# Performance work log

Hardware: AMD Instinct MI355X
Metric: run time of the kernel (lower is better)

## Reference

```python
import jax, jax.numpy as jnp
from jax import lax
import numpy as np

V, H = 512, 512


def gru_cell(x, h, Wih, Whh, bih, bhh):
    # PyTorch GRUCell: r,z,n gate order
    gi = x @ Wih.T + bih
    gh = h @ Whh.T + bhh
    ir, iz, inn = jnp.split(gi, 3, axis=-1)
    hr, hz, hn = jnp.split(gh, 3, axis=-1)
    r = jax.nn.sigmoid(ir + hr)
    z = jax.nn.sigmoid(iz + hz)
    n = jnp.tanh(inn + r * hn)
    return (1.0 - z) * n + z * h


def setup_inputs() -> dict:
    key = jax.random.key(0)
    ks = jax.random.split(key, 20)
    S, T, B = 200, 200, 256
    w = lambda k, shape: (jax.random.normal(k, shape, jnp.float32) * 0.05)
    inp = {
        "input_seq": jax.random.randint(ks[0], (S, B), 0, V),
        "input_len": jax.random.randint(ks[1], (B,), 1, S + 1),
        "target_seq": jax.random.randint(ks[2], (T, B), 0, V),
        "enc_embed": w(ks[3], (V, H)),
        "enc_Wih": w(ks[4], (3 * H, H)),
        "enc_Whh": w(ks[5], (3 * H, H)),
        "enc_bih": w(ks[6], (3 * H,)),
        "enc_bhh": w(ks[7], (3 * H,)),
        "att_W": w(ks[8], (H, H)),
        "att_b": w(ks[9], (H,)),
        "dec_embed": w(ks[10], (V, H)),
        "dec_Wih": w(ks[11], (3 * H, H)),
        "dec_Whh": w(ks[12], (3 * H, H)),
        "dec_bih": w(ks[13], (3 * H,)),
        "dec_bhh": w(ks[14], (3 * H,)),
        "mlp_W": w(ks[15], (H, 2 * H)),
        "mlp_b": w(ks[16], (H,)),
        "out_W": w(ks[17], (V, H)),
        "out_b": w(ks[18], (V,)),
    }
    return inp


def reference(input_seq, input_len, target_seq, enc_embed, enc_Wih, enc_Whh,
              enc_bih, enc_bhh, att_W, att_b, dec_embed, dec_Wih, dec_Whh,
              dec_bih, dec_bhh, mlp_W, mlp_b, out_W, out_b):
    S, B = input_seq.shape
    T = target_seq.shape[0]

    # ---- Encoder: length-masked GRU (equivalent to pack/pad) ----
    xs = enc_embed[input_seq]                              # (S,B,H)
    mask = jnp.arange(S)[:, None] < input_len[None, :]     # (S,B)
    h0 = jnp.zeros((B, H), xs.dtype)

    def estep(h, inp):
        x, m = inp
        m = m[:, None]
        hn = gru_cell(x, h, enc_Wih, enc_Whh, enc_bih, enc_bhh)
        h = jnp.where(m, hn, h)
        return h, jnp.where(m, h, 0.0)                     # padded outputs are zero

    h_enc, enc_out = lax.scan(estep, h0, (xs, mask))       # h_enc (B,H), enc_out (S,B,H)

    # ---- Decoder: teacher forcing (training path) ----
    dec_tokens = jnp.concatenate(
        [jnp.ones((1, B), target_seq.dtype), target_seq[:-1]], axis=0)  # start token 1
    dec_emb = dec_embed[dec_tokens]                        # (T,B,H)

    def dstep(h, emb_t):
        ah = jax.nn.relu(h @ att_W.T + att_b)              # (B,H)
        e = jnp.einsum('sbh,bh->bs', enc_out, ah)          # additive-style score
        att = jax.nn.softmax(e, axis=1)                    # (B,S)
        ctx = jnp.einsum('sbh,bs->bh', enc_out, att)       # (B,H)
        x = jnp.tanh(jnp.concatenate([emb_t, ctx], axis=1) @ mlp_W.T + mlp_b)
        hn = gru_cell(x, h, dec_Wih, dec_Whh, dec_bih, dec_bhh)
        dist = jax.nn.softmax(hn @ out_W.T + out_b, axis=1)
        return hn, dist

    _, dists = lax.scan(dstep, h_enc, dec_emb)             # (T,B,V)

    # ---- Loss: -log p[target] with clamp (== cal_loss) ----
    p = jnp.maximum(dists, 1e-10)
    tgt_p = jnp.take_along_axis(p, target_seq[:, :, None], axis=2)[..., 0]
    loss = jnp.mean(-jnp.log(tgt_p))

    # ---- Accuracy ----
    inference = jnp.argmax(dists, axis=-1)                 # (T,B)
    temacc = (inference == target_seq).astype(jnp.float32)
    all_acc = jnp.mean(temacc)
    acc = jnp.mean((jnp.sum(1.0 - temacc, axis=0) == 0).astype(jnp.float32))
    return inference.astype(jnp.float32), loss, acc, all_acc
```

## Files before the change

kernel.cpp:

```cpp
#include <hip/hip_runtime.h>
#include <math.h>

#define B 256
#define Hh 512
#define S 200
#define T 200
#define VOC 512
#define G3 1536
#define PAD 36

struct d4 { double x, y, z, w; };
__device__ __forceinline__ d4 tod4(const float4 a) {
    d4 r; r.x = a.x; r.y = a.y; r.z = a.z; r.w = a.w; return r;
}
__device__ __forceinline__ double dotd(const d4& a, const d4& b) {
    return a.x * b.x + a.y * b.y + a.z * b.z + a.w * b.w;
}
__device__ __forceinline__ double sigd(double x) { return 1.0 / (1.0 + exp(-x)); }

typedef double f64x4 __attribute__((ext_vector_type(4)));

__device__ __forceinline__ unsigned long long dbits(double v) {
    return (unsigned long long)__double_as_longlong(v);
}

__global__ __launch_bounds__(256) void gemm_at(
    const float* __restrict__ A,
    const float* __restrict__ W, int ldw, int woff,
    const float* __restrict__ bias,
    float* __restrict__ C, int ldc)
{
    __shared__ float As[32][PAD];
    __shared__ float Ws[32][PAD];
    const int tid = threadIdx.x;
    const int tx = tid & 15, ty = tid >> 4;
    const int j0 = blockIdx.x * 32, m0 = blockIdx.y * 32;
    const int lr = tid >> 3, lc = (tid & 7) * 4;

    double acc00 = 0.0, acc01 = 0.0, acc10 = 0.0, acc11 = 0.0;

    for (int k0 = 0; k0 < 512; k0 += 32) {
        float4 av = *(const float4*)(A + (size_t)(m0 + lr) * 512 + k0 + lc);
        float4 wv = *(const float4*)(W + (size_t)(j0 + lr) * ldw + woff + k0 + lc);
        __syncthreads();
        *(float4*)&As[lr][lc] = av;
        *(float4*)&Ws[lr][lc] = wv;
        __syncthreads();
#pragma unroll
        for (int kk = 0; kk < 32; kk += 4) {
            d4 a0 = tod4(*(const float4*)&As[ty][kk]);
            d4 a1 = tod4(*(const float4*)&As[ty + 16][kk]);
            d4 b0 = tod4(*(const float4*)&Ws[tx][kk]);
            d4 b1 = tod4(*(const float4*)&Ws[tx + 16][kk]);
            acc00 += dotd(a0, b0);
            acc01 += dotd(a0, b1);
            acc10 += dotd(a1, b0);
            acc11 += dotd(a1, b1);
        }
    }
    const int ms[2] = { m0 + ty, m0 + ty + 16 };
    const int js[2] = { j0 + tx, j0 + tx + 16 };
    double accs[2][2] = { { acc00, acc01 }, { acc10, acc11 } };
#pragma unroll
    for (int mi = 0; mi < 2; ++mi)
#pragma unroll
        for (int ji = 0; ji < 2; ++ji) {
            int m = ms[mi], j = js[ji];
            C[(size_t)m * ldc + j] = (float)(accs[mi][ji] + (double)bias[j]);
        }
}

__global__ __launch_bounds__(128) void gemm64(
    const float* __restrict__ A0, const float* __restrict__ A1,
    const float* __restrict__ W0, const float* __restrict__ W1,
    int split, int N, double* __restrict__ Csum,
    const int* __restrict__ ilen, int s)
{
    const int n0 = blockIdx.x * 64;
    const int m0 = blockIdx.y * 16;
    if (ilen) {
        int ml = 0;
        for (int i = 0; i < 16; ++i) ml = max(ml, ilen[m0 + i]);
        if (s >= ml) return;
    }
    __shared__ float As[16][516];
    __shared__ float Ws[64][68];
    const int tid = threadIdx.x;
    const bool lo = (n0 < split);
    const float* Ab = lo ? A0 : A1;
    const float* Wb = lo ? W0 : W1;
    const int nw = lo ? n0 : (n0 - split);

    const int lane = tid & 63;
    const int wv = tid >> 6;
    const int lr = lane & 15;
    const int g  = lane >> 4;

    f64x4 zf = { 0.0, 0.0, 0.0, 0.0 };
    f64x4 va = __builtin_amdgcn_mfma_f64_16x16x4f64(
        (double)(1ULL << lane), 1.0, zf, 0, 0, 0);
    const unsigned long long MM = 0xFFFFFFFFFFFFFULL;
    const unsigned long long M0 = (1ULL << 36) | (1ULL << 20) | (1ULL << 4);
    const int fam0 = __all(
        ((dbits(va[0]) & MM) == M0) && ((dbits(va[1]) & MM) == M0) &&
        ((dbits(va[2]) & MM) == M0) && ((dbits(va[3]) & MM) == M0));
    const int am = fam0 ? (lane & 15) : (lane >> 2);
    const int ak = fam0 ? (lane >> 4) : (lane & 3);
    f64x4 vr = __builtin_amdgcn_mfma_f64_16x16x4f64(
        (double)(1ULL << am), 1.0, zf, 0, 0, 0);

#pragma unroll 4
    for (int i = 0; i < 16; ++i) {
        *(float4*)&As[i][tid * 4] =
            *(const float4*)(Ab + (size_t)(m0 + i) * 512 + tid * 4);
    }

    float4 wreg[8];
#pragma unroll
    for (int i = 0; i < 8; ++i) {
        int x4 = i * 128 + tid, row = x4 >> 4, c4 = (x4 & 15) * 4;
        wreg[i] = *(const float4*)(Wb + (size_t)(nw + row) * 512 + c4);
    }
    __syncthreads();
#pragma unroll
    for (int i = 0; i < 8; ++i) {
        int x4 = i * 128 + tid, row = x4 >> 4, c4 = (x4 & 15) * 4;
        *(float4*)&Ws[row][c4] = wreg[i];
    }
    __syncthreads();

    const int nl0 = wv * 32;
    f64x4 c0 = { 0.0, 0.0, 0.0, 0.0 };
    f64x4 c1 = { 0.0, 0.0, 0.0, 0.0 };

    for (int k0 = 0; k0 < 512; k0 += 64) {
        const bool more = (k0 + 64) < 512;
        if (more) {
#pragma unroll
            for (int i = 0; i < 8; ++i) {
                int x4 = i * 128 + tid, row = x4 >> 4, c4 = (x4 & 15) * 4;
                wreg[i] = *(const float4*)(Wb + (size_t)(nw + row) * 512
                                           + k0 + 64 + c4);
            }
        }
#pragma unroll
        for (int kk = 0; kk < 16; ++kk) {
            double a  = (double)As[am][k0 + kk * 4 + ak];
            double b0 = (double)Ws[nl0 + lr][kk * 4 + g];
            double b1 = (double)Ws[nl0 + 16 + lr][kk * 4 + g];
            c0 = __builtin_amdgcn_mfma_f64_16x16x4f64(a, b0, c0, 0, 0, 0);
            c1 = __builtin_amdgcn_mfma_f64_16x16x4f64(a, b1, c1, 0, 0, 0);
        }
        __syncthreads();
        if (more) {
#pragma unroll
            for (int i = 0; i < 8; ++i) {
                int x4 = i * 128 + tid, row = x4 >> 4, c4 = (x4 & 15) * 4;
                *(float4*)&Ws[row][c4] = wreg[i];
            }
            __syncthreads();
        }
    }

#pragma unroll
    for (int d = 0; d < 4; ++d) {
        const int rowd = (int)((dbits(vr[d]) >> 52) & 0x7ff) - 1025;
        const size_t m = (size_t)(m0 + rowd);
        Csum[m * N + n0 + nl0 + lr]      = c0[d];
        Csum[m * N + n0 + nl0 + 16 + lr] = c1[d];
    }
}

__global__ __launch_bounds__(256) void enc_combine(
    const double* __restrict__ Csum,
    const float* __restrict__ h_in, float* __restrict__ h_out,
    const float* __restrict__ gi_tab, const int* __restrict__ iseq,
    const int* __restrict__ ilen, const float* __restrict__ bhh,
    int s, float* __restrict__ enc_out)
{
    const int idx = blockIdx.x * 256 + threadIdx.x;
    const int b = idx >> 9, j = idx & 511;
    const float hold = h_in[idx];
    float hnew = hold;
    if (s < ilen[b]) {
        const int tok = iseq[s * B + b];
        const float* gi = gi_tab + (size_t)tok * G3;
        const double* Cb = Csum + (size_t)b * 1536;
        double ar = Cb[j], az = Cb[512 + j], an = Cb[1024 + j];
        double r = sigd((double)gi[j] + ar + (double)bhh[j]);
        double z = sigd((double)gi[512 + j] + az + (double)bhh[512 + j]);
        double n = tanh((double)gi[1024 + j] + r * (an + (double)bhh[1024 + j]));
        hnew = (float)((1.0 - z) * n + z * (double)hold);
        enc_out[((size_t)s * B + b) * 512 + j] = hnew;
    } else {
        enc_out[((size_t)s * B + b) * 512 + j] = 0.f;
    }
    h_out[idx] = hnew;
}

__global__ __launch_bounds__(256) void proj_combine(
    const double* __restrict__ Csum,
    const float* __restrict__ att_b, const float* __restrict__ out_b,
    float* __restrict__ ah, float* __restrict__ logits, int t)
{
    const int idx = blockIdx.x * 256 + threadIdx.x;
    const int m = idx >> 10, n = idx & 1023;
    const double v = Csum[idx];
    if (n < 512) {
        if (t >= T) return;
        double r = v + (double)att_b[n]; if (r < 0.0) r = 0.0;
        ah[(size_t)m * 512 + n] = (float)r;
    } else {
        logits[(size_t)m * 512 + (n - 512)] = (float)(v + (double)out_b[n - 512]);
    }
}

__global__ __launch_bounds__(256) void dec_combine(
    const double* __restrict__ Csum,
    const float* __restrict__ bih, const float* __restrict__ bhh,
    const float* __restrict__ h_in, float* __restrict__ h_out)
{
    const int idx = blockIdx.x * 256 + threadIdx.x;
    const int b = idx >> 9, j = idx & 511;
    const double* Cb = Csum + (size_t)b * 3072;
    double air = Cb[j],        aiz = Cb[512 + j],  ain = Cb[1024 + j];
    double ahr = Cb[1536 + j], ahz = Cb[2048 + j], ahn = Cb[2560 + j];
    double r = sigd(air + (double)bih[j] + ahr + (double)bhh[j]);
    double z = sigd(aiz + (double)bih[512 + j] + ahz + (double)bhh[512 + j]);
    double n = tanh(ain + (double)bih[1024 + j] + r * (ahn + (double)bhh[1024 + j]));
    const float hold = h_in[idx];
    h_out[idx] = (float)((1.0 - z) * n + z * (double)hold);
}

__global__ __launch_bounds__(256) void attn_x_softmax(
    const float* __restrict__ enc_out, const float* __restrict__ ah,
    const float* __restrict__ mlp_W, const float* __restrict__ mlp_tab,
    const int* __restrict__ input_len, const int* __restrict__ target_seq,
    const float* __restrict__ logits, int t,
    float* __restrict__ xbuf, float* __restrict__ nll,
    float* __restrict__ inference)
{
    const int bid = blockIdx.x, tid = threadIdx.x;

    if (bid < B) {
        if (t >= T) return;
        __shared__ float scx[4][512];
        __shared__ double sml[8];
        __shared__ float ctxl[512];
        const int b = bid;
        const int wave = tid >> 6, lane = tid & 63;
        const int len = input_len[b];
        const float* ahb = ah + (size_t)b * 512;
        d4 aa1 = tod4(*(const float4*)(ahb + lane * 4));
        d4 aa2 = tod4(*(const float4*)(ahb + 256 + lane * 4));
        double m = -INFINITY, l = 0.0;
        d4 c1 = {0,0,0,0}, c2 = {0,0,0,0};
        for (int s = wave; s < len; s += 4) {
            const float* row = enc_out + ((size_t)s * B + b) * 512;
            d4 e1 = tod4(*(const float4*)(row + lane * 4));
            d4 e2 = tod4(*(const float4*)(row + 256 + lane * 4));
            double p = dotd(e1, aa1) + dotd(e2, aa2);
#pragma unroll
            for (int off = 32; off >= 1; off >>= 1) p += __shfl_xor(p, off, 64);
            double mn = fmax(m, p);
            double sc = (m == mn) ? 1.0 : exp(m - mn);
            double w = exp(p - mn);
            l = l * sc + w;
            c1.x = c1.x * sc + w * e1.x; c1.y = c1.y * sc + w * e1.y;
            c1.z = c1.z * sc + w * e1.z; c1.w = c1.w * sc + w * e1.w;
            c2.x = c2.x * sc + w * e2.x; c2.y = c2.y * sc + w * e2.y;
            c2.z = c2.z * sc + w * e2.z; c2.w = c2.w * sc + w * e2.w;
            m = mn;
        }
        if (lane == 0) { sml[wave] = m; sml[4 + wave] = l; }
        *(float4*)&scx[wave][lane * 4] =
            make_float4((float)c1.x, (float)c1.y, (float)c1.z, (float)c1.w);
        *(float4*)&scx[wave][256 + lane * 4] =
            make_float4((float)c2.x, (float)c2.y, (float)c2.z, (float)c2.w);
        __syncthreads();
        double M = fmax(fmax(sml[0], sml[1]), fmax(sml[2], sml[3]));
        if (len < S) M = fmax(M, 0.0);
        double w0 = exp(sml[0] - M), w1x = exp(sml[1] - M);
        double w2x = exp(sml[2] - M), w3 = exp(sml[3] - M);
        double L = sml[4] * w0 + sml[5] * w1x + sml[6] * w2x + sml[7] * w3
                 + (double)(S - len) * exp(0.0 - M);
        for (int jj = tid; jj < 512; jj += 256) {
            double v = (double)scx[0][jj] * w0 + (double)scx[1][jj] * w1x
                     + (double)scx[2][jj] * w2x + (double)scx[3][jj] * w3;
            ctxl[jj] = (float)(v / L);
        }
        __syncthreads();

        const int tok = (t == 0) ? 1 : target_seq[(t - 1) * B + b];
        const int q = tid & 3;
        const int rbase = tid >> 2;
#pragma unroll
        for (int pass = 0; pass < 8; ++pass) {
            const int jr = pass * 64 + rbase;
            const float* wr = mlp_W + (size_t)jr * 1024 + 512;
            double a = 0.0;
            for (int k = q * 4; k < 512; k += 16) {
                a += dotd(tod4(*(const float4*)&ctxl[k]),
                          tod4(*(const float4*)(wr + k)));
            }
            a += __shfl_xor(a, 1, 64);
            a += __shfl_xor(a, 2, 64);
            if (q == 0)
                xbuf[(size_t)b * 512 + jr] =
                    (float)tanh((double)mlp_tab[(size_t)tok * 512 + jr] + a);
        }
    } else {
        if (t < 1) return;
        __shared__ float red_f[256];
        __shared__ double red_d[256];
        __shared__ int red_i[256];
        const int sb = bid - B;
        const float* lg = logits + (size_t)sb * 512;
        const float l0 = lg[tid], l1 = lg[256 + tid];
        red_f[tid] = fmaxf(l0, l1);
        __syncthreads();
        for (int off = 128; off > 0; off >>= 1) {
            if (tid < off) red_f[tid] = fmaxf(red_f[tid], red_f[tid + off]);
            __syncthreads();
        }
        const double mx = (double)red_f[0];
        __syncthreads();
        const double e0 = exp((double)l0 - mx), e1 = exp((double)l1 - mx);
        red_d[tid] = e0 + e1;
        __syncthreads();
        for (int off = 128; off > 0; off >>= 1) {
            if (tid < off) red_d[tid] += red_d[tid + off];
            __syncthreads();
        }
        const double Z = red_d[0];
        __syncthreads();
        const float p0 = (float)(e0 / Z), p1 = (float)(e1 / Z);
        float v; int idx;
        if (p0 >= p1) { v = p0; idx = tid; } else { v = p1; idx = 256 + tid; }
        red_f[tid] = v; red_i[tid] = idx;
        __syncthreads();
        for (int off = 128; off > 0; off >>= 1) {
            if (tid < off) {
                float ov = red_f[tid + off]; int oi = red_i[tid + off];
                if (ov > red_f[tid] || (ov == red_f[tid] && oi < red_i[tid])) {
                    red_f[tid] = ov; red_i[tid] = oi;
                }
            }
            __syncthreads();
        }
        if (tid == 0) {
            int tg = target_seq[(t - 1) * B + sb];
            float pt = (float)(exp((double)lg[tg] - mx) / Z);
            pt = fmaxf(pt, 1e-10f);
            nll[(t - 1) * B + sb] = (float)(-log((double)pt));
            inference[(t - 1) * B + sb] = (float)red_i[0];
        }
    }
}

__global__ __launch_bounds__(256) void finalize_k(
    const float* __restrict__ nll, const float* __restrict__ inference,
    const int* __restrict__ target, float* __restrict__ out3)
{
    const int tid = threadIdx.x;
    int wrong = 0;
    double match = 0.0;
    const int b = tid;
    for (int t = 0; t < T; ++t) {
        float inf = inference[t * B + b];
        float tg = (float)target[t * B + b];
        bool ok = (inf == tg);
        match += ok ? 1.0 : 0.0;
        wrong |= !ok;
    }
    double lsum = 0.0;
    for (int i = tid; i < T * B; i += 256) lsum += (double)nll[i];

    __shared__ double sl[256], sm_[256], sa[256];
    sl[tid] = lsum; sm_[tid] = match; sa[tid] = wrong ? 0.0 : 1.0;
    __syncthreads();
    for (int off = 128; off > 0; off >>= 1) {
        if (tid < off) {
            sl[tid] += sl[tid + off];
            sm_[tid] += sm_[tid + off];
            sa[tid] += sa[tid + off];
        }
        __syncthreads();
    }
    if (tid == 0) {
        out3[0] = (float)(sl[0] / (double)(T * B));
        out3[1] = (float)(sa[0] / (double)B);
        out3[2] = (float)(sm_[0] / (double)(T * B));
    }
}

extern "C" void kernel_launch(void* const* d_in, const int* in_sizes, int n_in,
                              void* d_out, int out_size, void* d_ws, size_t ws_size,
                              hipStream_t stream)
{
    const int*   input_seq  = (const int*)d_in[0];
    const int*   input_len  = (const int*)d_in[1];
    const int*   target_seq = (const int*)d_in[2];
    const float* enc_embed  = (const float*)d_in[3];
    const float* enc_Wih    = (const float*)d_in[4];
    const float* enc_Whh    = (const float*)d_in[5];
    const float* enc_bih    = (const float*)d_in[6];
    const float* enc_bhh    = (const float*)d_in[7];
    const float* att_W      = (const float*)d_in[8];
    const float* att_b      = (const float*)d_in[9];
    const float* dec_embed  = (const float*)d_in[10];
    const float* dec_Wih    = (const float*)d_in[11];
    const float* dec_Whh    = (const float*)d_in[12];
    const float* dec_bih    = (const float*)d_in[13];
    const float* dec_bhh    = (const float*)d_in[14];
    const float* mlp_W      = (const float*)d_in[15];
    const float* mlp_b      = (const float*)d_in[16];
    const float* out_W      = (const float*)d_in[17];
    const float* out_b      = (const float*)d_in[18];

    float* out = (float*)d_out;

    float* gi_tab  = (float*)d_ws;
    float* mlp_tab = gi_tab + (size_t)VOC * G3;
    float* h0      = mlp_tab + (size_t)VOC * Hh;
    float* h1      = h0 + (size_t)B * Hh;
    float* ahb     = h1 + (size_t)B * Hh;
    float* xb      = ahb + (size_t)B * Hh;
    float* lgb     = xb + (size_t)B * Hh;
    float* nllb    = lgb + (size_t)B * Hh;
    float* enc_out = nllb + (size_t)T * B;
    double* gsum   = (double*)(enc_out + (size_t)S * B * Hh);

    hipMemsetAsync(h0, 0, (size_t)B * Hh * sizeof(float), stream);

    gemm_at<<<dim3(48, 16), 256, 0, stream>>>(
        enc_embed, enc_Wih, 512, 0, enc_bih, gi_tab, G3);
    gemm_at<<<dim3(16, 16), 256, 0, stream>>>(
        dec_embed, mlp_W, 1024, 0, mlp_b, mlp_tab, Hh);

    for (int s = 0; s < S; ++s) {
        const float* hc = (s & 1) ? h1 : h0;
        float* hx = (s & 1) ? h0 : h1;
        gemm64<<<dim3(24, 16), 128, 0, stream>>>(
            hc, hc, enc_Whh, enc_Whh, 1536, 1536, gsum, input_len, s);
        enc_combine<<<dim3(512), 256, 0, stream>>>(
            gsum, hc, hx, gi_tab, input_seq, input_len, enc_bhh, s, enc_out);
    }

    for (int t = 0; t <= T; ++t) {
        const float* hc = (t & 1) ? h1 : h0;
        float* hx = (t & 1) ? h0 : h1;
        gemm64<<<dim3(16, 16), 128, 0, stream>>>(
            hc, hc, att_W, out_W, 512, 1024, gsum, nullptr, 0);
        proj_combine<<<dim3(1024), 256, 0, stream>>>(
            gsum, att_b, out_b, ahb, lgb, t);
        attn_x_softmax<<<dim3(2 * B), 256, 0, stream>>>(
            enc_out, ahb, mlp_W, mlp_tab, input_len, target_seq,
            lgb, t, xb, nllb, out);
        if (t < T) {
            gemm64<<<dim3(48, 16), 128, 0, stream>>>(
                xb, hc, dec_Wih, dec_Whh, 1536, 3072, gsum, nullptr, 0);
            dec_combine<<<dim3(512), 256, 0, stream>>>(
                gsum, dec_bih, dec_bhh, hc, hx);
        }
    }

    finalize_k<<<dim3(1), 256, 0, stream>>>(nllb, out, target_seq, out + (size_t)T * B);
}
```

Baseline: 33.51 ms.

## Fuse GRU gate epilogues into MFMA GEMMs and merge decoder step kernels

```diff
diff --git a/kernel.cpp b/kernel.cpp
--- a/kernel.cpp
+++ b/kernel.cpp
@@ -22,6 +22,25 @@
 
 __device__ __forceinline__ unsigned long long dbits(double v) {
     return (unsigned long long)__double_as_longlong(v);
+}
+
+__device__ __forceinline__ void calib(int lane, int& am, int& ak, int* rowd)
+{
+    f64x4 z = { 0.0, 0.0, 0.0, 0.0 };
+    f64x4 va = __builtin_amdgcn_mfma_f64_16x16x4f64(
+        (double)(1ULL << lane), 1.0, z, 0, 0, 0);
+    const unsigned long long MM = 0xFFFFFFFFFFFFFULL;
+    const unsigned long long M0 = (1ULL << 36) | (1ULL << 20) | (1ULL << 4);
+    const int fam0 = __all(
+        ((dbits(va[0]) & MM) == M0) && ((dbits(va[1]) & MM) == M0) &&
+        ((dbits(va[2]) & MM) == M0) && ((dbits(va[3]) & MM) == M0));
+    am = fam0 ? (lane & 15) : (lane >> 2);
+    ak = fam0 ? (lane >> 4) : (lane & 3);
+    f64x4 vr = __builtin_amdgcn_mfma_f64_16x16x4f64(
+        (double)(1ULL << am), 1.0, z, 0, 0, 0);
+#pragma unroll
+    for (int d = 0; d < 4; ++d)
+        rowd[d] = (int)((dbits(vr[d]) >> 52) & 0x7ff) - 1025;
 }
 
 __global__ __launch_bounds__(256) void gemm_at(
@@ -70,189 +89,165 @@
         }
 }
 
-__global__ __launch_bounds__(128) void gemm64(
-    const float* __restrict__ A0, const float* __restrict__ A1,
-    const float* __restrict__ W0, const float* __restrict__ W1,
-    int split, int N, double* __restrict__ Csum,
-    const int* __restrict__ ilen, int s)
+__global__ __launch_bounds__(64) void enc_mfma(
+    const float* __restrict__ h_in, float* __restrict__ h_out,
+    const float* __restrict__ gi_tab, const int* __restrict__ iseq,
+    const int* __restrict__ ilen, const float* __restrict__ Whh,
+    const float* __restrict__ bhh, int s, float* __restrict__ enc_out)
 {
-    const int n0 = blockIdx.x * 64;
-    const int m0 = blockIdx.y * 16;
-    if (ilen) {
-        int ml = 0;
-        for (int i = 0; i < 16; ++i) ml = max(ml, ilen[m0 + i]);
-        if (s >= ml) return;
-    }
-    __shared__ float As[16][516];
+    const int lane = threadIdx.x;
+    const int j0 = blockIdx.x * 16, b0 = blockIdx.y * 16;
+
+    int ml = 0;
+    for (int i = 0; i < 16; ++i) ml = max(ml, ilen[b0 + i]);
+    if (s >= ml) {
+        for (int i = lane; i < 256; i += 64) {
+            int bq = b0 + (i >> 4), jq = j0 + (i & 15);
+            h_out[(size_t)bq * 512 + jq] = h_in[(size_t)bq * 512 + jq];
+            enc_out[((size_t)s * B + bq) * 512 + jq] = 0.f;
+        }
+        return;
+    }
+
     __shared__ float Ws[64][68];
-    const int tid = threadIdx.x;
-    const bool lo = (n0 < split);
-    const float* Ab = lo ? A0 : A1;
-    const float* Wb = lo ? W0 : W1;
-    const int nw = lo ? n0 : (n0 - split);
-
-    const int lane = tid & 63;
-    const int wv = tid >> 6;
-    const int lr = lane & 15;
-    const int g  = lane >> 4;
-
-    f64x4 zf = { 0.0, 0.0, 0.0, 0.0 };
-    f64x4 va = __builtin_amdgcn_mfma_f64_16x16x4f64(
-        (double)(1ULL << lane), 1.0, zf, 0, 0, 0);
-    const unsigned long long MM = 0xFFFFFFFFFFFFFULL;
-    const unsigned long long M0 = (1ULL << 36) | (1ULL << 20) | (1ULL << 4);
-    const int fam0 = __all(
-        ((dbits(va[0]) & MM) == M0) && ((dbits(va[1]) & MM) == M0) &&
-        ((dbits(va[2]) & MM) == M0) && ((dbits(va[3]) & MM) == M0));
-    const int am = fam0 ? (lane & 15) : (lane >> 2);
-    const int ak = fam0 ? (lane >> 4) : (lane & 3);
-    f64x4 vr = __builtin_amdgcn_mfma_f64_16x16x4f64(
-        (double)(1ULL << am), 1.0, zf, 0, 0, 0);
-
-#pragma unroll 4
+    const int lr = lane & 15, gk = lane >> 4;
+    int am, ak, rowd[4];
+    calib(lane, am, ak, rowd);
+
+    auto rowptr = [&](int r) -> const float* {
+        if (r < 48) return Whh + ((size_t)((r >> 4) * 512 + j0 + (r & 15))) * 512;
+        return h_in + (size_t)(b0 + r - 48) * 512;
+    };
+
+    float4 wreg[16];
+#pragma unroll
     for (int i = 0; i < 16; ++i) {
-        *(float4*)&As[i][tid * 4] =
-            *(const float4*)(Ab + (size_t)(m0 + i) * 512 + tid * 4);
-    }
-
-    float4 wreg[8];
-#pragma unroll
-    for (int i = 0; i < 8; ++i) {
-        int x4 = i * 128 + tid, row = x4 >> 4, c4 = (x4 & 15) * 4;
-        wreg[i] = *(const float4*)(Wb + (size_t)(nw + row) * 512 + c4);
+        int x4 = i * 64 + lane, row = x4 >> 4, c4 = (x4 & 15) * 4;
+        wreg[i] = *(const float4*)(rowptr(row) + c4);
+    }
+#pragma unroll
+    for (int i = 0; i < 16; ++i) {
+        int x4 = i * 64 + lane, row = x4 >> 4, c4 = (x4 & 15) * 4;
+        *(float4*)&Ws[row][c4] = wreg[i];
     }
     __syncthreads();
-#pragma unroll
-    for (int i = 0; i < 8; ++i) {
-        int x4 = i * 128 + tid, row = x4 >> 4, c4 = (x4 & 15) * 4;
-        *(float4*)&Ws[row][c4] = wreg[i];
-    }
-    __syncthreads();
-
-    const int nl0 = wv * 32;
-    f64x4 c0 = { 0.0, 0.0, 0.0, 0.0 };
-    f64x4 c1 = { 0.0, 0.0, 0.0, 0.0 };
-
+
+    f64x4 c0 = {0,0,0,0}, c1 = {0,0,0,0}, c2 = {0,0,0,0};
     for (int k0 = 0; k0 < 512; k0 += 64) {
         const bool more = (k0 + 64) < 512;
         if (more) {
 #pragma unroll
-            for (int i = 0; i < 8; ++i) {
-                int x4 = i * 128 + tid, row = x4 >> 4, c4 = (x4 & 15) * 4;
-                wreg[i] = *(const float4*)(Wb + (size_t)(nw + row) * 512
-                                           + k0 + 64 + c4);
+            for (int i = 0; i < 16; ++i) {
+                int x4 = i * 64 + lane, row = x4 >> 4, c4 = (x4 & 15) * 4;
+                wreg[i] = *(const float4*)(rowptr(row) + k0 + 64 + c4);
             }
         }
 #pragma unroll
         for (int kk = 0; kk < 16; ++kk) {
-            double a  = (double)As[am][k0 + kk * 4 + ak];
-            double b0 = (double)Ws[nl0 + lr][kk * 4 + g];
-            double b1 = (double)Ws[nl0 + 16 + lr][kk * 4 + g];
-            c0 = __builtin_amdgcn_mfma_f64_16x16x4f64(a, b0, c0, 0, 0, 0);
-            c1 = __builtin_amdgcn_mfma_f64_16x16x4f64(a, b1, c1, 0, 0, 0);
+            double a  = (double)Ws[48 + am][kk * 4 + ak];
+            double br = (double)Ws[lr][kk * 4 + gk];
+            double bz = (double)Ws[16 + lr][kk * 4 + gk];
+            double bn = (double)Ws[32 + lr][kk * 4 + gk];
+            c0 = __builtin_amdgcn_mfma_f64_16x16x4f64(a, br, c0, 0, 0, 0);
+            c1 = __builtin_amdgcn_mfma_f64_16x16x4f64(a, bz, c1, 0, 0, 0);
+            c2 = __builtin_amdgcn_mfma_f64_16x16x4f64(a, bn, c2, 0, 0, 0);
         }
         __syncthreads();
         if (more) {
 #pragma unroll
-            for (int i = 0; i < 8; ++i) {
-                int x4 = i * 128 + tid, row = x4 >> 4, c4 = (x4 & 15) * 4;
+            for (int i = 0; i < 16; ++i) {
+                int x4 = i * 64 + lane, row = x4 >> 4, c4 = (x4 & 15) * 4;
                 *(float4*)&Ws[row][c4] = wreg[i];
             }
             __syncthreads();
         }
     }
 
+    const int j = j0 + lr;
 #pragma unroll
     for (int d = 0; d < 4; ++d) {
-        const int rowd = (int)((dbits(vr[d]) >> 52) & 0x7ff) - 1025;
-        const size_t m = (size_t)(m0 + rowd);
-        Csum[m * N + n0 + nl0 + lr]      = c0[d];
-        Csum[m * N + n0 + nl0 + 16 + lr] = c1[d];
-    }
-}
-
-__global__ __launch_bounds__(256) void enc_combine(
-    const double* __restrict__ Csum,
-    const float* __restrict__ h_in, float* __restrict__ h_out,
-    const float* __restrict__ gi_tab, const int* __restrict__ iseq,
-    const int* __restrict__ ilen, const float* __restrict__ bhh,
-    int s, float* __restrict__ enc_out)
-{
-    const int idx = blockIdx.x * 256 + threadIdx.x;
-    const int b = idx >> 9, j = idx & 511;
-    const float hold = h_in[idx];
-    float hnew = hold;
-    if (s < ilen[b]) {
-        const int tok = iseq[s * B + b];
-        const float* gi = gi_tab + (size_t)tok * G3;
-        const double* Cb = Csum + (size_t)b * 1536;
-        double ar = Cb[j], az = Cb[512 + j], an = Cb[1024 + j];
-        double r = sigd((double)gi[j] + ar + (double)bhh[j]);
-        double z = sigd((double)gi[512 + j] + az + (double)bhh[512 + j]);
-        double n = tanh((double)gi[1024 + j] + r * (an + (double)bhh[1024 + j]));
-        hnew = (float)((1.0 - z) * n + z * (double)hold);
-        enc_out[((size_t)s * B + b) * 512 + j] = hnew;
-    } else {
-        enc_out[((size_t)s * B + b) * 512 + j] = 0.f;
-    }
-    h_out[idx] = hnew;
-}
-
-__global__ __launch_bounds__(256) void proj_combine(
-    const double* __restrict__ Csum,
-    const float* __restrict__ att_b, const float* __restrict__ out_b,
-    float* __restrict__ ah, float* __restrict__ logits, int t)
-{
-    const int idx = blockIdx.x * 256 + threadIdx.x;
-    const int m = idx >> 10, n = idx & 1023;
-    const double v = Csum[idx];
-    if (n < 512) {
-        if (t >= T) return;
-        double r = v + (double)att_b[n]; if (r < 0.0) r = 0.0;
-        ah[(size_t)m * 512 + n] = (float)r;
-    } else {
-        logits[(size_t)m * 512 + (n - 512)] = (float)(v + (double)out_b[n - 512]);
-    }
-}
-
-__global__ __launch_bounds__(256) void dec_combine(
-    const double* __restrict__ Csum,
-    const float* __restrict__ bih, const float* __restrict__ bhh,
-    const float* __restrict__ h_in, float* __restrict__ h_out)
-{
-    const int idx = blockIdx.x * 256 + threadIdx.x;
-    const int b = idx >> 9, j = idx & 511;
-    const double* Cb = Csum + (size_t)b * 3072;
-    double air = Cb[j],        aiz = Cb[512 + j],  ain = Cb[1024 + j];
-    double ahr = Cb[1536 + j], ahz = Cb[2048 + j], ahn = Cb[2560 + j];
-    double r = sigd(air + (double)bih[j] + ahr + (double)bhh[j]);
-    double z = sigd(aiz + (double)bih[512 + j] + ahz + (double)bhh[512 + j]);
-    double n = tanh(ain + (double)bih[1024 + j] + r * (ahn + (double)bhh[1024 + j]));
-    const float hold = h_in[idx];
-    h_out[idx] = (float)((1.0 - z) * n + z * (double)hold);
-}
-
-__global__ __launch_bounds__(256) void attn_x_softmax(
-    const float* __restrict__ enc_out, const float* __restrict__ ah,
+        const int b = b0 + rowd[d];
+        float hold = h_in[(size_t)b * 512 + j];
+        float hnew = hold;
+        if (s < ilen[b]) {
+            int tok = iseq[s * B + b];
+            const float* gi = gi_tab + (size_t)tok * G3;
+            double r = sigd((double)gi[j] + c0[d] + (double)bhh[j]);
+            double z = sigd((double)gi[512 + j] + c1[d] + (double)bhh[512 + j]);
+            double n = tanh((double)gi[1024 + j] + r * (c2[d] + (double)bhh[1024 + j]));
+            hnew = (float)((1.0 - z) * n + z * (double)hold);
+            enc_out[((size_t)s * B + b) * 512 + j] = hnew;
+        } else {
+            enc_out[((size_t)s * B + b) * 512 + j] = 0.f;
+        }
+        h_out[(size_t)b * 512 + j] = hnew;
+    }
+}
+
+union K1sm {
+    struct {
+        float scx[4][512];
+        float ctxl[512];
+        float hl[512];
+        float ah_l[512];
+        double sml[8];
+    } a;
+    struct {
+        float red_f[256];
+        double red_d[256];
+        int red_i[256];
+    } s;
+    struct {
+        float As[16][68];
+        float Ws[64][68];
+    } g;
+};
+
+__global__ __launch_bounds__(256) void dec_att(
+    const float* __restrict__ enc_out, const float* __restrict__ h,
+    const float* __restrict__ att_W, const float* __restrict__ att_b,
+    const float* __restrict__ out_W, const float* __restrict__ out_b,
     const float* __restrict__ mlp_W, const float* __restrict__ mlp_tab,
     const int* __restrict__ input_len, const int* __restrict__ target_seq,
-    const float* __restrict__ logits, int t,
+    float* __restrict__ lgbA, const float* __restrict__ lgbB, int t,
     float* __restrict__ xbuf, float* __restrict__ nll,
     float* __restrict__ inference)
 {
+    __shared__ K1sm sm;
     const int bid = blockIdx.x, tid = threadIdx.x;
 
     if (bid < B) {
         if (t >= T) return;
-        __shared__ float scx[4][512];
-        __shared__ double sml[8];
-        __shared__ float ctxl[512];
         const int b = bid;
+        for (int i = tid; i < 128; i += 256)
+            *(float4*)&sm.a.hl[i * 4] =
+                *(const float4*)(h + (size_t)b * 512 + i * 4);
+        __syncthreads();
+        {
+            const int q = tid & 3, rbase = tid >> 2;
+#pragma unroll
+            for (int pass = 0; pass < 8; ++pass) {
+                const int jr = pass * 64 + rbase;
+                const float* wr = att_W + (size_t)jr * 512;
+                double a = 0.0;
+                for (int k = q * 4; k < 512; k += 16)
+                    a += dotd(tod4(*(const float4*)&sm.a.hl[k]),
+                              tod4(*(const float4*)(wr + k)));
+                a += __shfl_xor(a, 1, 64);
+                a += __shfl_xor(a, 2, 64);
+                if (q == 0) {
+                    double v = a + (double)att_b[jr];
+                    if (v < 0.0) v = 0.0;
+                    sm.a.ah_l[jr] = (float)v;
+                }
+            }
+        }
+        __syncthreads();
+
         const int wave = tid >> 6, lane = tid & 63;
         const int len = input_len[b];
-        const float* ahb = ah + (size_t)b * 512;
-        d4 aa1 = tod4(*(const float4*)(ahb + lane * 4));
-        d4 aa2 = tod4(*(const float4*)(ahb + 256 + lane * 4));
+        d4 aa1 = tod4(*(const float4*)&sm.a.ah_l[lane * 4]);
+        d4 aa2 = tod4(*(const float4*)&sm.a.ah_l[256 + lane * 4]);
         double m = -INFINITY, l = 0.0;
         d4 c1 = {0,0,0,0}, c2 = {0,0,0,0};
         for (int s = wave; s < len; s += 4) {
@@ -272,22 +267,23 @@
             c2.z = c2.z * sc + w * e2.z; c2.w = c2.w * sc + w * e2.w;
             m = mn;
         }
-        if (lane == 0) { sml[wave] = m; sml[4 + wave] = l; }
-        *(float4*)&scx[wave][lane * 4] =
+        if (lane == 0) { sm.a.sml[wave] = m; sm.a.sml[4 + wave] = l; }
+        *(float4*)&sm.a.scx[wave][lane * 4] =
             make_float4((float)c1.x, (float)c1.y, (float)c1.z, (float)c1.w);
-        *(float4*)&scx[wave][256 + lane * 4] =
+        *(float4*)&sm.a.scx[wave][256 + lane * 4] =
             make_float4((float)c2.x, (float)c2.y, (float)c2.z, (float)c2.w);
         __syncthreads();
-        double M = fmax(fmax(sml[0], sml[1]), fmax(sml[2], sml[3]));
+        double M = fmax(fmax(sm.a.sml[0], sm.a.sml[1]),
+                        fmax(sm.a.sml[2], sm.a.sml[3]));
         if (len < S) M = fmax(M, 0.0);
-        double w0 = exp(sml[0] - M), w1x = exp(sml[1] - M);
-        double w2x = exp(sml[2] - M), w3 = exp(sml[3] - M);
-        double L = sml[4] * w0 + sml[5] * w1x + sml[6] * w2x + sml[7] * w3
-                 + (double)(S - len) * exp(0.0 - M);
+        double w0 = exp(sm.a.sml[0] - M), w1x = exp(sm.a.sml[1] - M);
+        double w2x = exp(sm.a.sml[2] - M), w3 = exp(sm.a.sml[3] - M);
+        double L = sm.a.sml[4] * w0 + sm.a.sml[5] * w1x + sm.a.sml[6] * w2x
+                 + sm.a.sml[7] * w3 + (double)(S - len) * exp(0.0 - M);
         for (int jj = tid; jj < 512; jj += 256) {
-            double v = (double)scx[0][jj] * w0 + (double)scx[1][jj] * w1x
-                     + (double)scx[2][jj] * w2x + (double)scx[3][jj] * w3;
-            ctxl[jj] = (float)(v / L);
+            double v = (double)sm.a.scx[0][jj] * w0 + (double)sm.a.scx[1][jj] * w1x
+                     + (double)sm.a.scx[2][jj] * w2x + (double)sm.a.scx[3][jj] * w3;
+            sm.a.ctxl[jj] = (float)(v / L);
         }
         __syncthreads();
 
@@ -300,7 +296,7 @@
             const float* wr = mlp_W + (size_t)jr * 1024 + 512;
             double a = 0.0;
             for (int k = q * 4; k < 512; k += 16) {
-                a += dotd(tod4(*(const float4*)&ctxl[k]),
+                a += dotd(tod4(*(const float4*)&sm.a.ctxl[k]),
                           tod4(*(const float4*)(wr + k)));
             }
             a += __shfl_xor(a, 1, 64);
@@ -309,51 +305,211 @@
                 xbuf[(size_t)b * 512 + jr] =
                     (float)tanh((double)mlp_tab[(size_t)tok * 512 + jr] + a);
         }
-    } else {
-        if (t < 1) return;
-        __shared__ float red_f[256];
-        __shared__ double red_d[256];
-        __shared__ int red_i[256];
+    } else if (bid < 2 * B) {
+        if (t < 2) return;
         const int sb = bid - B;
-        const float* lg = logits + (size_t)sb * 512;
+        const int dt = t - 2;
+        const float* lg = lgbB + (size_t)sb * 512;
         const float l0 = lg[tid], l1 = lg[256 + tid];
-        red_f[tid] = fmaxf(l0, l1);
+        sm.s.red_f[tid] = fmaxf(l0, l1);
         __syncthreads();
         for (int off = 128; off > 0; off >>= 1) {
-            if (tid < off) red_f[tid] = fmaxf(red_f[tid], red_f[tid + off]);
+            if (tid < off)
+                sm.s.red_f[tid] = fmaxf(sm.s.red_f[tid], sm.s.red_f[tid + off]);
             __syncthreads();
         }
-        const double mx = (double)red_f[0];
+        const double mx = (double)sm.s.red_f[0];
         __syncthreads();
         const double e0 = exp((double)l0 - mx), e1 = exp((double)l1 - mx);
-        red_d[tid] = e0 + e1;
+        sm.s.red_d[tid] = e0 + e1;
         __syncthreads();
         for (int off = 128; off > 0; off >>= 1) {
-            if (tid < off) red_d[tid] += red_d[tid + off];
+            if (tid < off) sm.s.red_d[tid] += sm.s.red_d[tid + off];
             __syncthreads();
         }
-        const double Z = red_d[0];
+        const double Z = sm.s.red_d[0];
         __syncthreads();
         const float p0 = (float)(e0 / Z), p1 = (float)(e1 / Z);
         float v; int idx;
         if (p0 >= p1) { v = p0; idx = tid; } else { v = p1; idx = 256 + tid; }
-        red_f[tid] = v; red_i[tid] = idx;
+        sm.s.red_f[tid] = v; sm.s.red_i[tid] = idx;
         __syncthreads();
         for (int off = 128; off > 0; off >>= 1) {
             if (tid < off) {
-                float ov = red_f[tid + off]; int oi = red_i[tid + off];
-                if (ov > red_f[tid] || (ov == red_f[tid] && oi < red_i[tid])) {
-                    red_f[tid] = ov; red_i[tid] = oi;
+                float ov = sm.s.red_f[tid + off]; int oi = sm.s.red_i[tid + off];
+                if (ov > sm.s.red_f[tid] ||
+                    (ov == sm.s.red_f[tid] && oi < sm.s.red_i[tid])) {
+                    sm.s.red_f[tid] = ov; sm.s.red_i[tid] = oi;
                 }
             }
             __syncthreads();
         }
         if (tid == 0) {
-            int tg = target_seq[(t - 1) * B + sb];
+            int tg = target_seq[dt * B + sb];
             float pt = (float)(exp((double)lg[tg] - mx) / Z);
             pt = fmaxf(pt, 1e-10f);
-            nll[(t - 1) * B + sb] = (float)(-log((double)pt));
-            inference[(t - 1) * B + sb] = (float)red_i[0];
+            nll[dt * B + sb] = (float)(-log((double)pt));
+            inference[dt * B + sb] = (float)sm.s.red_i[0];
+        }
+    } else {
+        if (t < 1 || t > T) return;
+        const int g = bid - 2 * B;
+        const int n0 = (g & 7) * 64, m0 = (g >> 3) * 16;
+        const int lane = tid & 63, wv = tid >> 6;
+        const int lr = lane & 15, gk = lane >> 4;
+        int am, ak, rowd[4];
+        calib(lane, am, ak, rowd);
+
+        const int arow = tid >> 4, ac4 = (tid & 15) * 4;
+        float4 areg = *(const float4*)(h + (size_t)(m0 + arow) * 512 + ac4);
+        float4 wreg[4];
+#pragma unroll
+        for (int i = 0; i < 4; ++i) {
+            int x4 = i * 256 + tid, row = x4 >> 4, c4 = (x4 & 15) * 4;
+            wreg[i] = *(const float4*)(out_W + (size_t)(n0 + row) * 512 + c4);
+        }
+        *(float4*)&sm.g.As[arow][ac4] = areg;
+#pragma unroll
+        for (int i = 0; i < 4; ++i) {
+            int x4 = i * 256 + tid, row = x4 >> 4, c4 = (x4 & 15) * 4;
+            *(float4*)&sm.g.Ws[row][c4] = wreg[i];
+        }
+        __syncthreads();
+
+        f64x4 c = {0,0,0,0};
+        for (int k0 = 0; k0 < 512; k0 += 64) {
+            const bool more = (k0 + 64) < 512;
+            if (more) {
+                areg = *(const float4*)(h + (size_t)(m0 + arow) * 512
+                                        + k0 + 64 + ac4);
+#pragma unroll
+                for (int i = 0; i < 4; ++i) {
+                    int x4 = i * 256 + tid, row = x4 >> 4, c4 = (x4 & 15) * 4;
+                    wreg[i] = *(const float4*)(out_W + (size_t)(n0 + row) * 512
+                                               + k0 + 64 + c4);
+                }
+            }
+#pragma unroll
+            for (int kk = 0; kk < 16; ++kk) {
+                double a  = (double)sm.g.As[am][kk * 4 + ak];
+                double bb = (double)sm.g.Ws[wv * 16 + lr][kk * 4 + gk];
+                c = __builtin_amdgcn_mfma_f64_16x16x4f64(a, bb, c, 0, 0, 0);
+            }
+            __syncthreads();
+            if (more) {
+                *(float4*)&sm.g.As[arow][ac4] = areg;
+#pragma unroll
+                for (int i = 0; i < 4; ++i) {
+                    int x4 = i * 256 + tid, row = x4 >> 4, c4 = (x4 & 15) * 4;
+                    *(float4*)&sm.g.Ws[row][c4] = wreg[i];
+                }
+                __syncthreads();
+            }
+        }
+        const int ng = n0 + wv * 16 + lr;
+#pragma unroll
+        for (int d = 0; d < 4; ++d)
+            lgbA[(size_t)(m0 + rowd[d]) * 512 + ng] =
+                (float)(c[d] + (double)out_b[ng]);
+    }
+}
+
+__global__ __launch_bounds__(128) void dec_gru2(
+    const float* __restrict__ x, const float* __restrict__ h_in,
+    const float* __restrict__ Wih, const float* __restrict__ Whh,
+    const float* __restrict__ bih, const float* __restrict__ bhh,
+    float* __restrict__ h_out)
+{
+    __shared__ float Ws[128][68];
+    __shared__ double Lx[3][4][64];
+    const int tid = threadIdx.x;
+    const int lane = tid & 63, wv = tid >> 6;
+    const int j0 = blockIdx.x * 16, b0 = blockIdx.y * 16;
+    const int lr = lane & 15, gk = lane >> 4;
+    int am, ak, rowd[4];
+    calib(lane, am, ak, rowd);
+
+    auto rowptr = [&](int r) -> const float* {
+        if (r < 48)
+            return Wih + ((size_t)((r >> 4) * 512 + j0 + (r & 15))) * 512;
+        if (r < 96) {
+            int rr = r - 48;
+            return Whh + ((size_t)((rr >> 4) * 512 + j0 + (rr & 15))) * 512;
+        }
+        if (r < 112) return x + (size_t)(b0 + r - 96) * 512;
+        return h_in + (size_t)(b0 + r - 112) * 512;
+    };
+
+    float4 wreg[16];
+#pragma unroll
+    for (int i = 0; i < 16; ++i) {
+        int x4 = i * 128 + tid, row = x4 >> 4, c4 = (x4 & 15) * 4;
+        wreg[i] = *(const float4*)(rowptr(row) + c4);
+    }
+#pragma unroll
+    for (int i = 0; i < 16; ++i) {
+        int x4 = i * 128 + tid, row = x4 >> 4, c4 = (x4 & 15) * 4;
+        *(float4*)&Ws[row][c4] = wreg[i];
+    }
+    __syncthreads();
+
+    const int ab = 96 + wv * 16;
+    const int bb = wv * 48;
+    f64x4 c0 = {0,0,0,0}, c1 = {0,0,0,0}, c2 = {0,0,0,0};
+
+    for (int k0 = 0; k0 < 512; k0 += 64) {
+        const bool more = (k0 + 64) < 512;
+        if (more) {
+#pragma unroll
+            for (int i = 0; i < 16; ++i) {
+                int x4 = i * 128 + tid, row = x4 >> 4, c4 = (x4 & 15) * 4;
+                wreg[i] = *(const float4*)(rowptr(row) + k0 + 64 + c4);
+            }
+        }
+#pragma unroll
+        for (int kk = 0; kk < 16; ++kk) {
+            double a  = (double)Ws[ab + am][kk * 4 + ak];
+            double br = (double)Ws[bb + lr][kk * 4 + gk];
+            double bz = (double)Ws[bb + 16 + lr][kk * 4 + gk];
+            double bn = (double)Ws[bb + 32 + lr][kk * 4 + gk];
+            c0 = __builtin_amdgcn_mfma_f64_16x16x4f64(a, br, c0, 0, 0, 0);
+            c1 = __builtin_amdgcn_mfma_f64_16x16x4f64(a, bz, c1, 0, 0, 0);
+            c2 = __builtin_amdgcn_mfma_f64_16x16x4f64(a, bn, c2, 0, 0, 0);
+        }
+        __syncthreads();
+        if (more) {
+#pragma unroll
+            for (int i = 0; i < 16; ++i) {
+                int x4 = i * 128 + tid, row = x4 >> 4, c4 = (x4 & 15) * 4;
+                *(float4*)&Ws[row][c4] = wreg[i];
+            }
+            __syncthreads();
+        }
+    }
+
+    if (wv == 1) {
+#pragma unroll
+        for (int d = 0; d < 4; ++d) {
+            Lx[0][d][lane] = c0[d];
+            Lx[1][d][lane] = c1[d];
+            Lx[2][d][lane] = c2[d];
+        }
+    }
+    __syncthreads();
+    if (wv == 0) {
+        const int j = j0 + lr;
+#pragma unroll
+        for (int d = 0; d < 4; ++d) {
+            const int b = b0 + rowd[d];
+            double air = c0[d], aiz = c1[d], ain = c2[d];
+            double ahr = Lx[0][d][lane], ahz = Lx[1][d][lane],
+                   ahn = Lx[2][d][lane];
+            double r = sigd(air + (double)bih[j] + ahr + (double)bhh[j]);
+            double z = sigd(aiz + (double)bih[512 + j] + ahz + (double)bhh[512 + j]);
+            double n = tanh(ain + (double)bih[1024 + j]
+                            + r * (ahn + (double)bhh[1024 + j]));
+            float hold = h_in[(size_t)b * 512 + j];
+            h_out[(size_t)b * 512 + j] = (float)((1.0 - z) * n + z * (double)hold);
         }
     }
 }
@@ -424,12 +580,11 @@
     float* mlp_tab = gi_tab + (size_t)VOC * G3;
     float* h0      = mlp_tab + (size_t)VOC * Hh;
     float* h1      = h0 + (size_t)B * Hh;
-    float* ahb     = h1 + (size_t)B * Hh;
-    float* xb      = ahb + (size_t)B * Hh;
-    float* lgb     = xb + (size_t)B * Hh;
-    float* nllb    = lgb + (size_t)B * Hh;
+    float* lgb_odd = h1 + (size_t)B * Hh;
+    float* xb      = lgb_odd + (size_t)B * Hh;
+    float* lgb_evn = xb + (size_t)B * Hh;
+    float* nllb    = lgb_evn + (size_t)B * Hh;
     float* enc_out = nllb + (size_t)T * B;
-    double* gsum   = (double*)(enc_out + (size_t)S * B * Hh);
 
     hipMemsetAsync(h0, 0, (size_t)B * Hh * sizeof(float), stream);
 
@@ -441,27 +596,21 @@
     for (int s = 0; s < S; ++s) {
         const float* hc = (s & 1) ? h1 : h0;
         float* hx = (s & 1) ? h0 : h1;
-        gemm64<<<dim3(24, 16), 128, 0, stream>>>(
-            hc, hc, enc_Whh, enc_Whh, 1536, 1536, gsum, input_len, s);
-        enc_combine<<<dim3(512), 256, 0, stream>>>(
-            gsum, hc, hx, gi_tab, input_seq, input_len, enc_bhh, s, enc_out);
-    }
-
-    for (int t = 0; t <= T; ++t) {
+        enc_mfma<<<dim3(32, 16), 64, 0, stream>>>(
+            hc, hx, gi_tab, input_seq, input_len, enc_Whh, enc_bhh, s, enc_out);
+    }
+
+    for (int t = 0; t <= T + 1; ++t) {
         const float* hc = (t & 1) ? h1 : h0;
         float* hx = (t & 1) ? h0 : h1;
-        gemm64<<<dim3(16, 16), 128, 0, stream>>>(
-            hc, hc, att_W, out_W, 512, 1024, gsum, nullptr, 0);
-        proj_combine<<<dim3(1024), 256, 0, stream>>>(
-            gsum, att_b, out_b, ahb, lgb, t);
-        attn_x_softmax<<<dim3(2 * B), 256, 0, stream>>>(
-            enc_out, ahb, mlp_W, mlp_tab, input_len, target_seq,
-            lgb, t, xb, nllb, out);
+        float* lgbA = (t & 1) ? lgb_odd : lgb_evn;
+        const float* lgbB = (t & 1) ? lgb_evn : lgb_odd;
+        dec_att<<<dim3(640), 256, 0, stream>>>(
+            enc_out, hc, att_W, att_b, out_W, out_b, mlp_W, mlp_tab,
+            input_len, target_seq, lgbA, lgbB, t, xb, nllb, out);
         if (t < T) {
-            gemm64<<<dim3(48, 16), 128, 0, stream>>>(
-                xb, hc, dec_Wih, dec_Whh, 1536, 3072, gsum, nullptr, 0);
-            dec_combine<<<dim3(512), 256, 0, stream>>>(
-                gsum, dec_bih, dec_bhh, hc, hx);
+            dec_gru2<<<dim3(32, 16), 128, 0, stream>>>(
+                xb, hc, dec_Wih, dec_Whh, dec_bih, dec_bhh, hx);
         }
     }
 
```

Result: slower. 44.91 ms (+34.0%).
